# Optimization experiments

Measured on AMD Instinct MI355X. Metric: run time of the kernel, lower is better.

The kernel has to match this reference:

```python
import jax, jax.numpy as jnp
import numpy as np

N, E, D, H = 8192, 262144, 128, 64


def setup_inputs() -> dict:
    key = jax.random.key(0)
    ks = jax.random.split(key, 6)
    edge_index = jax.random.randint(ks[0], (2, E), 0, N, dtype=jnp.int64)
    adj = jnp.zeros((N, N), jnp.float32).at[edge_index[0], edge_index[1]].set(1.0)
    embed = jax.random.normal(ks[1], (N, D), jnp.float32)
    noise = jax.random.uniform(ks[2], (E,), jnp.float32, minval=1e-6, maxval=1.0 - 1e-6)
    W1 = jax.random.normal(ks[3], (2 * D, H), jnp.float32) / np.float32(np.sqrt(2 * D))
    b1 = jnp.zeros((H,), jnp.float32)
    W2 = jax.random.normal(ks[4], (H, 1), jnp.float32) / np.float32(np.sqrt(H))
    b2 = jnp.zeros((1,), jnp.float32)
    return {"embed": embed, "adj": adj, "noise": noise, "W1": W1, "b1": b1,
            "W2": W2, "b2": b2, "edge_index": edge_index}


def reference(embed, adj, noise, W1, b1, W2, b2, edge_index):
    row, col = edge_index[0], edge_index[1]
    # edge gather + concat: [E, 2D]
    h = jnp.concatenate([embed[row], embed[col]], axis=-1)
    # elayers: Linear(2D,64) -> ReLU -> Linear(64,1)
    log_alpha = (jax.nn.relu(h @ W1 + b1) @ W2 + b2).reshape(-1)  # [E]
    # concrete sigmoid sampling, beta (tmp) = 1.0
    gate = jax.nn.sigmoid(jnp.log(noise) - jnp.log1p(-noise) + log_alpha)
    # sparse COO build + coalesce (sum duplicates) + to_dense
    n = adj.shape[0]
    mask = jnp.zeros((n, n), adj.dtype).at[row, col].add(gate)
    # symmetrize and apply adjacency
    sym = 0.5 * (mask + mask.T)
    masked_adj = adj * sym
    return masked_adj
```

## Files before the change

kernel.cpp:

```cpp
#include <hip/hip_runtime.h>
#include <hip/hip_bf16.h>

#define NN 8192
#define EE 262144
#define DD 128
#define HH 64

__global__ void init_kernel(const float* __restrict__ embed,
                            const float* __restrict__ W1,
                            const int* __restrict__ ei,
                            float* __restrict__ Pt,
                            float* __restrict__ Pb,
                            int* __restrict__ flag,
                            float4* __restrict__ out4) {
    const int tid  = threadIdx.x;
    const int w    = tid >> 6;
    const int lane = tid & 63;

    const float4 z = make_float4(0.f, 0.f, 0.f, 0.f);
    const size_t base = (size_t)blockIdx.x * 8192 + tid;
#pragma unroll
    for (int i = 0; i < 32; ++i)
        out4[base + (size_t)i * 256] = z;

    if (blockIdx.x == 0 && tid < 64) {
        int v = ei[2 * tid + 1];
        unsigned long long b = __ballot(v != 0);
        if (tid == 0) flag[0] = (b == 0ULL) ? 1 : 0;
    }

    __shared__ float esh[4][DD];
    const int n = (blockIdx.x << 2) + w;
    esh[w][lane]      = embed[n * DD + lane];
    esh[w][lane + 64] = embed[n * DD + 64 + lane];
    __syncthreads();

    float at = 0.f, ab = 0.f;
#pragma unroll 8
    for (int k = 0; k < DD; ++k) {
        float ek = esh[w][k];
        at = fmaf(ek, W1[k * HH + lane],        at);
        ab = fmaf(ek, W1[(DD + k) * HH + lane], ab);
    }
    Pt[n * HH + lane] = at;
    Pb[n * HH + lane] = ab;
}

__global__ void edge_kernel(const float4* __restrict__ Pt4,
                            const float4* __restrict__ Pb4,
                            const float* __restrict__ b1,
                            const float* __restrict__ W2,
                            const float* __restrict__ b2,
                            const float* __restrict__ noise,
                            const int* __restrict__ ei,
                            const int* __restrict__ flag,
                            const float* __restrict__ adj,
                            float* __restrict__ out) {
    const int tid  = threadIdx.x;
    const int lane = tid & 63;
    const int q    = lane & 15;
    const int gw   = (blockIdx.x << 2) + (tid >> 6);
    const int e    = (gw << 2) + (lane >> 4);

    int r, c;
    if (flag[0]) {
        r = ei[2 * e];
        c = ei[2 * (EE + e)];
    } else {
        r = ei[e];
        c = ei[EE + e];
    }

    const float4 pt = Pt4[r * 16 + q];
    const float4 pb = Pb4[c * 16 + q];
    const float4 bb = ((const float4*)b1)[q];
    const float4 ww = ((const float4*)W2)[q];

    float v = fmaxf(pt.x + pb.x + bb.x, 0.f) * ww.x
            + fmaxf(pt.y + pb.y + bb.y, 0.f) * ww.y
            + fmaxf(pt.z + pb.z + bb.z, 0.f) * ww.z
            + fmaxf(pt.w + pb.w + bb.w, 0.f) * ww.w;

#pragma unroll
    for (int off = 8; off; off >>= 1) v += __shfl_xor(v, off, 64);

    if (q == 0) {
        const float la    = v + b2[0];
        const float u     = noise[e];
        const float logit = logf(u) - log1pf(-u) + la;
        const float g2    = 0.5f / (1.f + expf(-logit));

        const size_t rc = (size_t)r * NN + c;
        const size_t cr = (size_t)c * NN + r;
        atomicAdd(&out[rc], g2);
        const float a = adj[cr];
        if (a != 0.f) atomicAdd(&out[cr], g2 * a);
    }
}

extern "C" void kernel_launch(void* const* d_in, const int* in_sizes, int n_in,
                              void* d_out, int out_size, void* d_ws, size_t ws_size,
                              hipStream_t stream) {
    const float* embed = (const float*)d_in[0];
    const float* adj   = (const float*)d_in[1];
    const float* noise = (const float*)d_in[2];
    const float* W1    = (const float*)d_in[3];
    const float* b1    = (const float*)d_in[4];
    const float* W2    = (const float*)d_in[5];
    const float* b2    = (const float*)d_in[6];
    const int*   ei    = (const int*)d_in[7];
    float* out = (float*)d_out;

    float* Pt = (float*)d_ws;
    float* Pb = Pt + (size_t)NN * HH;
    int* flag = (int*)((char*)d_ws + 2ull * NN * HH * sizeof(float));

    init_kernel<<<NN / 4, 256, 0, stream>>>(embed, W1, ei, Pt, Pb, flag,
                                            (float4*)out);
    edge_kernel<<<EE / 16, 256, 0, stream>>>((const float4*)Pt, (const float4*)Pb,
                                             b1, W2, b2, noise, ei, flag, adj, out);
}
```

Before: 452.8 us.

## Split zero-fill into separate blocks and process four edges per 16-lane group

The init kernel now runs separate blocks that only zero the 256 MB output, instead of making each projection block also zero 8192 float4s. The edge kernel has each 16-lane group handle four edges, batching the gathers and the noise and adj loads for more memory-level parallelism. The int64 index-format check moves into each edge block as a per-block shared flag, which removes the global flag. Each edge block now re-reads the edge indices for this check and uses more registers.

```diff
diff --git a/kernel.cpp b/kernel.cpp
--- a/kernel.cpp
+++ b/kernel.cpp
@@ -6,31 +6,32 @@
 #define DD 128
 #define HH 64
 
+#define PRE_BLOCKS  2048
+#define FILL_BLOCKS 8192
+#define EPW 16
+
 __global__ void init_kernel(const float* __restrict__ embed,
                             const float* __restrict__ W1,
-                            const int* __restrict__ ei,
                             float* __restrict__ Pt,
                             float* __restrict__ Pb,
-                            int* __restrict__ flag,
                             float4* __restrict__ out4) {
-    const int tid  = threadIdx.x;
+    const int tid = threadIdx.x;
+    const int b   = blockIdx.x;
+
+    if (b >= PRE_BLOCKS) {
+        const size_t base = (size_t)(b - PRE_BLOCKS) * 2048 + tid;
+        const float4 z = make_float4(0.f, 0.f, 0.f, 0.f);
+#pragma unroll
+        for (int i = 0; i < 8; ++i)
+            out4[base + (size_t)i * 256] = z;
+        return;
+    }
+
     const int w    = tid >> 6;
     const int lane = tid & 63;
-
-    const float4 z = make_float4(0.f, 0.f, 0.f, 0.f);
-    const size_t base = (size_t)blockIdx.x * 8192 + tid;
-#pragma unroll
-    for (int i = 0; i < 32; ++i)
-        out4[base + (size_t)i * 256] = z;
-
-    if (blockIdx.x == 0 && tid < 64) {
-        int v = ei[2 * tid + 1];
-        unsigned long long b = __ballot(v != 0);
-        if (tid == 0) flag[0] = (b == 0ULL) ? 1 : 0;
-    }
+    const int n    = (b << 2) + w;
 
     __shared__ float esh[4][DD];
-    const int n = (blockIdx.x << 2) + w;
     esh[w][lane]      = embed[n * DD + lane];
     esh[w][lane + 64] = embed[n * DD + 64 + lane];
     __syncthreads();
@@ -53,48 +54,77 @@
                             const float* __restrict__ b2,
                             const float* __restrict__ noise,
                             const int* __restrict__ ei,
-                            const int* __restrict__ flag,
                             const float* __restrict__ adj,
                             float* __restrict__ out) {
     const int tid  = threadIdx.x;
     const int lane = tid & 63;
     const int q    = lane & 15;
-    const int gw   = (blockIdx.x << 2) + (tid >> 6);
-    const int e    = (gw << 2) + (lane >> 4);
+    const int g16  = lane >> 4;
 
-    int r, c;
-    if (flag[0]) {
-        r = ei[2 * e];
-        c = ei[2 * (EE + e)];
+    __shared__ int sflag;
+    if (tid < 64) {
+        int v = ei[2 * tid + 1];
+        unsigned long long bal = __ballot(v != 0);
+        if (tid == 0) sflag = (bal == 0ULL) ? 1 : 0;
+    }
+    __syncthreads();
+    const bool i64 = (sflag != 0);
+
+    const int wav   = (blockIdx.x << 2) + (tid >> 6);
+    const int ebase = wav * EPW + g16 * 4;
+
+    int r[4], c[4];
+    if (i64) {
+#pragma unroll
+        for (int i = 0; i < 4; ++i) {
+            r[i] = ei[2 * (ebase + i)];
+            c[i] = ei[2 * (EE + ebase + i)];
+        }
     } else {
-        r = ei[e];
-        c = ei[EE + e];
+#pragma unroll
+        for (int i = 0; i < 4; ++i) {
+            r[i] = ei[ebase + i];
+            c[i] = ei[EE + ebase + i];
+        }
     }
 
-    const float4 pt = Pt4[r * 16 + q];
-    const float4 pb = Pb4[c * 16 + q];
     const float4 bb = ((const float4*)b1)[q];
     const float4 ww = ((const float4*)W2)[q];
 
-    float v = fmaxf(pt.x + pb.x + bb.x, 0.f) * ww.x
-            + fmaxf(pt.y + pb.y + bb.y, 0.f) * ww.y
-            + fmaxf(pt.z + pb.z + bb.z, 0.f) * ww.z
-            + fmaxf(pt.w + pb.w + bb.w, 0.f) * ww.w;
+    float v[4];
+#pragma unroll
+    for (int i = 0; i < 4; ++i) {
+        const float4 pt = Pt4[r[i] * 16 + q];
+        const float4 pb = Pb4[c[i] * 16 + q];
+        v[i] = fmaxf(pt.x + pb.x + bb.x, 0.f) * ww.x
+             + fmaxf(pt.y + pb.y + bb.y, 0.f) * ww.y
+             + fmaxf(pt.z + pb.z + bb.z, 0.f) * ww.z
+             + fmaxf(pt.w + pb.w + bb.w, 0.f) * ww.w;
+    }
 
 #pragma unroll
-    for (int off = 8; off; off >>= 1) v += __shfl_xor(v, off, 64);
+    for (int i = 0; i < 4; ++i)
+#pragma unroll
+        for (int off = 8; off; off >>= 1)
+            v[i] += __shfl_xor(v[i], off, 64);
 
     if (q == 0) {
-        const float la    = v + b2[0];
-        const float u     = noise[e];
-        const float logit = logf(u) - log1pf(-u) + la;
-        const float g2    = 0.5f / (1.f + expf(-logit));
-
-        const size_t rc = (size_t)r * NN + c;
-        const size_t cr = (size_t)c * NN + r;
-        atomicAdd(&out[rc], g2);
-        const float a = adj[cr];
-        if (a != 0.f) atomicAdd(&out[cr], g2 * a);
+        const float bias2 = b2[0];
+        float u[4], a[4];
+#pragma unroll
+        for (int i = 0; i < 4; ++i) {
+            u[i] = noise[ebase + i];
+            a[i] = adj[(size_t)c[i] * NN + r[i]];
+        }
+#pragma unroll
+        for (int i = 0; i < 4; ++i) {
+            const float la    = v[i] + bias2;
+            const float logit = logf(u[i]) - log1pf(-u[i]) + la;
+            const float g2    = 0.5f / (1.f + expf(-logit));
+            atomicAdd(&out[(size_t)r[i] * NN + c[i]], g2);
+            if (a[i] != 0.f)
+                atomicAdd(&out[(size_t)c[i] * NN + r[i]], g2 * a[i]);
+        }
     }
 }
 
@@ -113,10 +143,9 @@
 
     float* Pt = (float*)d_ws;
     float* Pb = Pt + (size_t)NN * HH;
-    int* flag = (int*)((char*)d_ws + 2ull * NN * HH * sizeof(float));
 
-    init_kernel<<<NN / 4, 256, 0, stream>>>(embed, W1, ei, Pt, Pb, flag,
-                                            (float4*)out);
-    edge_kernel<<<EE / 16, 256, 0, stream>>>((const float4*)Pt, (const float4*)Pb,
-                                             b1, W2, b2, noise, ei, flag, adj, out);
+    init_kernel<<<PRE_BLOCKS + FILL_BLOCKS, 256, 0, stream>>>(
+        embed, W1, Pt, Pb, (float4*)out);
+    edge_kernel<<<EE / (EPW * 4), 256, 0, stream>>>(
+        (const float4*)Pt, (const float4*)Pb, b1, W2, b2, noise, ei, adj, out);
 }
```

Result: no change. 448.7 us (-0.9%).
